# Kernel tuning notes

Measured on AMD Instinct MI355X. Metric: run time of the kernel, lower is better.

## Reference

```python
import jax, jax.numpy as jnp
import numpy as np

B = 16      # number of point clouds
N = 4096    # points per cloud (max after densify)
D = 3       # xyz


def setup_inputs() -> dict:
    key = jax.random.key(0)
    k1, k2 = jax.random.split(key)
    pred = jax.random.normal(k1, (B * N, D), dtype=jnp.float32)
    target = jax.random.normal(k2, (B * N, D), dtype=jnp.float32)
    # sorted segment ids, equal-sized clouds (faithful to to_dense_batch usage)
    batch = jnp.repeat(jnp.arange(B, dtype=jnp.int64), N)
    return {"pred": pred, "target": target, "batch": batch}


def to_dense_batch(x, batch, num_batches, max_n):
    # PyG to_dense_batch: scatter flat points into [B, max_n, D], zero-padded.
    ones = jnp.ones_like(batch)
    counts = jax.ops.segment_sum(ones, batch, num_segments=num_batches)
    offsets = jnp.concatenate([jnp.zeros((1,), batch.dtype), jnp.cumsum(counts)[:-1]])
    pos = jnp.arange(batch.shape[0], dtype=batch.dtype) - offsets[batch]
    dense = jnp.zeros((num_batches, max_n, x.shape[-1]), x.dtype)
    return dense.at[batch, pos].set(x)


def chamfer_distance(x, y):
    # squared-euclidean pairwise distances via the GEMM identity
    x2 = jnp.sum(x * x, axis=-1)                      # [B, N]
    y2 = jnp.sum(y * y, axis=-1)                      # [B, M]
    xy = jnp.einsum('bnd,bmd->bnm', x, y)             # [B, N, M]
    d = x2[:, :, None] + y2[:, None, :] - 2.0 * xy    # [B, N, M]
    cham_x = jnp.mean(jnp.min(d, axis=2), axis=1)     # mean over N of min over M
    cham_y = jnp.mean(jnp.min(d, axis=1), axis=1)     # mean over M of min over N
    # point_reduction='mean', batch_reduction='mean' (pytorch3d defaults)
    return jnp.mean(cham_x + cham_y)


def reference(pred, target, batch):
    x = to_dense_batch(pred, batch, B, N)
    y = to_dense_batch(target, batch, B, N)
    return chamfer_distance(x, y)
```

## Files before the change

kernel.cpp:

```cpp
#include <hip/hip_runtime.h>


namespace {

constexpr int kB = 16;
constexpr int kN = 4096;
constexpr int kPlane = kB * kN;
constexpr int kJS = 2;
constexpr int kJSL = kN / kJS;
constexpr float kScale = 1.0f / (float)(kB * kN);

typedef short bf16x8 __attribute__((ext_vector_type(8)));
typedef float f32x16 __attribute__((ext_vector_type(16)));
typedef unsigned short u16;

__device__ inline u16 bf16_rn(float f) {
  union { float f; unsigned u; } v; v.f = f;
  unsigned r = v.u + 0x7fffu + ((v.u >> 16) & 1u);
  return (u16)(r >> 16);
}
__device__ inline float bf16_f(u16 h) {
  union { unsigned u; float f; } v; v.u = (unsigned)h << 16;
  return v.f;
}
__device__ inline unsigned pk2(u16 lo, u16 hi) {
  return (unsigned)lo | ((unsigned)hi << 16);
}

__global__ void init_out(float* out) { out[0] = 0.0f; }

__global__ __launch_bounds__(256) void cd_prep(
    const float* __restrict__ pred, const float* __restrict__ targ,
    u16* __restrict__ Ab, u16* __restrict__ Bb, float* __restrict__ out) {
  const int p = blockIdx.x * 256 + threadIdx.x;
  if (p == 0) out[0] = 0.0f;
  const u16 one = 0x3F80;
  {
    const float a = pred[3 * p], c = pred[3 * p + 1], d = pred[3 * p + 2];
    const u16 ah = bf16_rn(a), ch = bf16_rn(c), dh = bf16_rn(d);
    const u16 al = bf16_rn(a - bf16_f(ah));
    const u16 cl = bf16_rn(c - bf16_f(ch));
    const u16 dl = bf16_rn(d - bf16_f(dh));
    const float s2 = fmaf(a, a, fmaf(c, c, d * d));
    const u16 s2h = bf16_rn(s2);
    const u16 s2l = bf16_rn(s2 - bf16_f(s2h));
    uint4 w0, w1;
    w0.x = pk2(ah, ch); w0.y = pk2(dh, al); w0.z = pk2(cl, dl); w0.w = pk2(ah, ch);
    w1.x = pk2(dh, s2h); w1.y = pk2(s2l, one); w1.z = pk2(one, al); w1.w = pk2(cl, dl);
    uint4* dst = reinterpret_cast<uint4*>(Ab + (size_t)p * 16);
    dst[0] = w0; dst[1] = w1;
  }
  {
    const float a = targ[3 * p], c = targ[3 * p + 1], d = targ[3 * p + 2];
    const u16 ah0 = bf16_rn(a), ch0 = bf16_rn(c), dh0 = bf16_rn(d);
    const u16 ah = bf16_rn(-2.0f * bf16_f(ah0));
    const u16 ch = bf16_rn(-2.0f * bf16_f(ch0));
    const u16 dh = bf16_rn(-2.0f * bf16_f(dh0));
    const u16 al = bf16_rn(-2.0f * bf16_f(bf16_rn(a - bf16_f(ah0))));
    const u16 cl = bf16_rn(-2.0f * bf16_f(bf16_rn(c - bf16_f(ch0))));
    const u16 dl = bf16_rn(-2.0f * bf16_f(bf16_rn(d - bf16_f(dh0))));
    const float s2 = fmaf(a, a, fmaf(c, c, d * d));
    const u16 s2h = bf16_rn(s2);
    const u16 s2l = bf16_rn(s2 - bf16_f(s2h));
    uint4 w0, w1;
    w0.x = pk2(ah, ch); w0.y = pk2(dh, ah); w0.z = pk2(ch, dh); w0.w = pk2(al, cl);
    w1.x = pk2(dl, one); w1.y = pk2(one, s2h); w1.z = pk2(s2l, al); w1.w = pk2(cl, dl);
    uint4* dst = reinterpret_cast<uint4*>(Bb + (size_t)p * 16);
    dst[0] = w0; dst[1] = w1;
  }
}

__global__ __launch_bounds__(256) void cd_rowmin(
    const u16* __restrict__ Ab, const u16* __restrict__ Bb,
    float* __restrict__ rowpart) {
  const int t = threadIdx.x;
  const int w = t >> 6, lane = t & 63;
  const int half = lane >> 5, l31 = lane & 31;
  const int chunk = blockIdx.x;
  const int cloud = blockIdx.y;
  const int z = blockIdx.z;
  const int dir = z / kJS;
  const int slice = z % kJS;

  const u16* __restrict__ RowM = dir ? Bb : Ab;
  const u16* __restrict__ ColM = dir ? Ab : Bb;

  const int arow = cloud * kN + chunk * 128 + w * 32 + l31;
  const bf16x8 afrag = *(const bf16x8*)(RowM + (size_t)arow * 16 + half * 8);

  f32x16 zacc;
#pragma unroll
  for (int r = 0; r < 16; ++r) zacc[r] = 0.0f;
  float rmin[16];
#pragma unroll
  for (int r = 0; r < 16; ++r) rmin[r] = 1e30f;

  const u16* bbase = ColM + ((size_t)cloud * kN + slice * kJSL) * 16;
  constexpr int NT = kJSL / 64;
  const int jcol = l31 * 16 + half * 8;
#pragma unroll 2
  for (int jt = 0; jt < NT; ++jt) {
    const u16* bp = bbase + jt * 64 * 16;
    const bf16x8 b0 = *(const bf16x8*)(bp + jcol);
    const bf16x8 b1 = *(const bf16x8*)(bp + 32 * 16 + jcol);
    const f32x16 s0 = __builtin_amdgcn_mfma_f32_32x32x16_bf16(afrag, b0, zacc, 0, 0, 0);
    const f32x16 s1 = __builtin_amdgcn_mfma_f32_32x32x16_bf16(afrag, b1, zacc, 0, 0, 0);
#pragma unroll
    for (int r = 0; r < 16; ++r)
      rmin[r] = fminf(rmin[r], fminf(s0[r], s1[r]));
  }

#pragma unroll
  for (int st = 1; st < 32; st <<= 1) {
#pragma unroll
    for (int r = 0; r < 16; ++r)
      rmin[r] = fminf(rmin[r], __shfl_xor(rmin[r], st, 64));
  }
  if (l31 == 0) {
    float* rp = rowpart + ((size_t)z * kB + cloud) * kN + chunk * 128 + w * 32;
#pragma unroll
    for (int r = 0; r < 16; ++r) {
      const int row = (r & 3) + 8 * (r >> 2) + 4 * half;
      rp[row] = rmin[r];
    }
  }
}

__global__ __launch_bounds__(256) void cd_reduce(
    const float* __restrict__ rowpart, float* __restrict__ out) {
  const int u = blockIdx.x * 256 + threadIdx.x;
  const int dir = u >> 16, rest = u & (kPlane - 1);
  const int cloud = rest >> 12, p = rest & (kN - 1);
  float rm = 1e30f;
#pragma unroll
  for (int s2 = 0; s2 < kJS; ++s2)
    rm = fminf(rm, rowpart[(((size_t)(dir * kJS + s2)) * kB + cloud) * kN + p]);
  float s = rm;
  for (int o = 32; o > 0; o >>= 1) s += __shfl_down(s, o, 64);
  __shared__ float wsum[4];
  const int lane = threadIdx.x & 63, wv = threadIdx.x >> 6;
  if (lane == 0) wsum[wv] = s;
  __syncthreads();
  if (threadIdx.x == 0)
    atomicAdd(out, (wsum[0] + wsum[1] + wsum[2] + wsum[3]) * kScale);
}

template <int KX>
__global__ __launch_bounds__(256) void chamfer_direct(
    const float* __restrict__ pred, const float* __restrict__ targ,
    float* __restrict__ out) {
  __shared__ float4 tA[128], tB[128];
  const int t = threadIdx.x;
  const int xb = blockIdx.x, b = blockIdx.y, dir = blockIdx.z;
  const float* __restrict__ X = dir ? targ : pred;
  const float* __restrict__ Y = dir ? pred : targ;
  float2 xx2[KX], xy2[KX], xz2[KX];
  float x2[KX], mn[KX];
  const int ibase = b * kN + xb * (256 * KX) + t;
#pragma unroll
  for (int k = 0; k < KX; ++k) {
    const int i = ibase + k * 256;
    const float a = X[3 * i], c = X[3 * i + 1], d = X[3 * i + 2];
    x2[k] = fmaf(a, a, fmaf(c, c, d * d));
    xx2[k] = make_float2(-2.0f * a, -2.0f * a);
    xy2[k] = make_float2(-2.0f * c, -2.0f * c);
    xz2[k] = make_float2(-2.0f * d, -2.0f * d);
    mn[k] = 1e30f;
  }
  for (int t0 = 0; t0 < kN; t0 += 256) {
    __syncthreads();
    if (t < 128) {
      const int j0 = 3 * (b * kN + t0 + 2 * t);
      const float a0 = Y[j0], c0 = Y[j0 + 1], d0 = Y[j0 + 2];
      const float a1 = Y[j0 + 3], c1 = Y[j0 + 4], d1 = Y[j0 + 5];
      tA[t] = make_float4(a0, a1, c0, c1);
      tB[t] = make_float4(d0, d1, fmaf(a0, a0, fmaf(c0, c0, d0 * d0)),
                          fmaf(a1, a1, fmaf(c1, c1, d1 * d1)));
    }
    __syncthreads();
    for (int jj = 0; jj < 128; ++jj) {
      const float4 qa = tA[jj], qb = tB[jj];
      const float2 qx = make_float2(qa.x, qa.y), qy = make_float2(qa.z, qa.w);
      const float2 qz = make_float2(qb.x, qb.y), qw = make_float2(qb.z, qb.w);
#pragma unroll
      for (int k = 0; k < KX; ++k) {
        float2 acc;
        asm("v_pk_fma_f32 %0, %1, %2, %3\n\t"
            "v_pk_fma_f32 %0, %4, %5, %0\n\t"
            "v_pk_fma_f32 %0, %6, %7, %0"
            : "=&v"(acc)
            : "v"(xz2[k]), "v"(qz), "v"(qw), "v"(xy2[k]), "v"(qy),
              "v"(xx2[k]), "v"(qx));
        asm("v_min3_f32 %0, %0, %1, %2" : "+v"(mn[k]) : "v"(acc.x), "v"(acc.y));
      }
    }
  }
  float s = 0.0f;
#pragma unroll
  for (int k = 0; k < KX; ++k) s += x2[k] + mn[k];
  for (int o = 32; o > 0; o >>= 1) s += __shfl_down(s, o, 64);
  __shared__ float wsum[4];
  const int lane = t & 63, wv = t >> 6;
  if (lane == 0) wsum[wv] = s;
  __syncthreads();
  if (t == 0)
    atomicAdd(out, (wsum[0] + wsum[1] + wsum[2] + wsum[3]) * kScale);
}

}

extern "C" void kernel_launch(void* const* d_in, const int* in_sizes, int n_in,
                              void* d_out, int out_size, void* d_ws,
                              size_t ws_size, hipStream_t stream) {
  const float* pred = (const float*)d_in[0];
  const float* targ = (const float*)d_in[1];
  float* out = (float*)d_out;

  const size_t needA = (size_t)kPlane * 16 * sizeof(u16);
  const size_t needRow = (size_t)2 * kJS * kPlane * sizeof(float);
  if (ws_size >= 2 * needA + needRow) {
    u16* Ab = (u16*)d_ws;
    u16* Bb = (u16*)((char*)d_ws + needA);
    float* rowpart = (float*)((char*)d_ws + 2 * needA);
    cd_prep<<<dim3(kPlane / 256), 256, 0, stream>>>(pred, targ, Ab, Bb, out);
    cd_rowmin<<<dim3(32, kB, 2 * kJS), 256, 0, stream>>>(Ab, Bb, rowpart);
    cd_reduce<<<dim3(2 * kPlane / 256), 256, 0, stream>>>(rowpart, out);
  } else {
    init_out<<<dim3(1), dim3(1), 0, stream>>>(out);
    constexpr int KX = 8;
    dim3 grid(kN / (256 * KX), kB, 2);
    chamfer_direct<KX><<<grid, 256, 0, stream>>>(pred, targ, out);
  }
}
```

Before: 114.1 us.

## Register-block four A fragments per wave and split columns across waves

Each wave now holds four 32-row A fragments and walks a quarter of the column points, so every B fragment it loads feeds eight MFMAs where it previously fed two. The two-way column slicing across the grid is replaced by a four-way split across the waves of a block, which halves the grid and doubles the rowpart buffer read by the reduce kernel. This cuts global B traffic per MFMA at the cost of 64 accumulator registers of running minima per lane plus MFMA result registers, which may lower occupancy, and the loop-unroll pragma is dropped.

```diff
diff --git a/kernel.cpp b/kernel.cpp
--- a/kernel.cpp
+++ b/kernel.cpp
@@ -6,8 +6,8 @@
 constexpr int kB = 16;
 constexpr int kN = 4096;
 constexpr int kPlane = kB * kN;
-constexpr int kJS = 2;
-constexpr int kJSL = kN / kJS;
+constexpr int kQ = 4;
+constexpr int kQL = kN / kQ;
 constexpr float kScale = 1.0f / (float)(kB * kN);
 
 typedef short bf16x8 __attribute__((ext_vector_type(8)));
@@ -78,51 +78,64 @@
   const int half = lane >> 5, l31 = lane & 31;
   const int chunk = blockIdx.x;
   const int cloud = blockIdx.y;
-  const int z = blockIdx.z;
-  const int dir = z / kJS;
-  const int slice = z % kJS;
+  const int dir = blockIdx.z;
 
   const u16* __restrict__ RowM = dir ? Bb : Ab;
   const u16* __restrict__ ColM = dir ? Ab : Bb;
 
-  const int arow = cloud * kN + chunk * 128 + w * 32 + l31;
-  const bf16x8 afrag = *(const bf16x8*)(RowM + (size_t)arow * 16 + half * 8);
+  bf16x8 af[4];
+#pragma unroll
+  for (int a = 0; a < 4; ++a) {
+    const int arow = cloud * kN + chunk * 128 + a * 32 + l31;
+    af[a] = *(const bf16x8*)(RowM + (size_t)arow * 16 + half * 8);
+  }
 
   f32x16 zacc;
 #pragma unroll
   for (int r = 0; r < 16; ++r) zacc[r] = 0.0f;
-  float rmin[16];
-#pragma unroll
-  for (int r = 0; r < 16; ++r) rmin[r] = 1e30f;
-
-  const u16* bbase = ColM + ((size_t)cloud * kN + slice * kJSL) * 16;
-  constexpr int NT = kJSL / 64;
+  float rmin[4][16];
+#pragma unroll
+  for (int a = 0; a < 4; ++a)
+#pragma unroll
+    for (int r = 0; r < 16; ++r) rmin[a][r] = 1e30f;
+
+  const u16* bbase = ColM + ((size_t)cloud * kN + w * kQL) * 16;
+  constexpr int NT = kQL / 64;
   const int jcol = l31 * 16 + half * 8;
-#pragma unroll 2
   for (int jt = 0; jt < NT; ++jt) {
     const u16* bp = bbase + jt * 64 * 16;
     const bf16x8 b0 = *(const bf16x8*)(bp + jcol);
     const bf16x8 b1 = *(const bf16x8*)(bp + 32 * 16 + jcol);
-    const f32x16 s0 = __builtin_amdgcn_mfma_f32_32x32x16_bf16(afrag, b0, zacc, 0, 0, 0);
-    const f32x16 s1 = __builtin_amdgcn_mfma_f32_32x32x16_bf16(afrag, b1, zacc, 0, 0, 0);
-#pragma unroll
-    for (int r = 0; r < 16; ++r)
-      rmin[r] = fminf(rmin[r], fminf(s0[r], s1[r]));
+#pragma unroll
+    for (int a = 0; a < 4; ++a) {
+      const f32x16 s0 =
+          __builtin_amdgcn_mfma_f32_32x32x16_bf16(af[a], b0, zacc, 0, 0, 0);
+      const f32x16 s1 =
+          __builtin_amdgcn_mfma_f32_32x32x16_bf16(af[a], b1, zacc, 0, 0, 0);
+#pragma unroll
+      for (int r = 0; r < 16; ++r)
+        rmin[a][r] = fminf(rmin[a][r], fminf(s0[r], s1[r]));
+    }
   }
 
 #pragma unroll
   for (int st = 1; st < 32; st <<= 1) {
 #pragma unroll
-    for (int r = 0; r < 16; ++r)
-      rmin[r] = fminf(rmin[r], __shfl_xor(rmin[r], st, 64));
+    for (int a = 0; a < 4; ++a)
+#pragma unroll
+      for (int r = 0; r < 16; ++r)
+        rmin[a][r] = fminf(rmin[a][r], __shfl_xor(rmin[a][r], st, 64));
   }
   if (l31 == 0) {
-    float* rp = rowpart + ((size_t)z * kB + cloud) * kN + chunk * 128 + w * 32;
-#pragma unroll
-    for (int r = 0; r < 16; ++r) {
-      const int row = (r & 3) + 8 * (r >> 2) + 4 * half;
-      rp[row] = rmin[r];
-    }
+    float* rp =
+        rowpart + (((size_t)dir * kQ + w) * kB + cloud) * kN + chunk * 128;
+#pragma unroll
+    for (int a = 0; a < 4; ++a)
+#pragma unroll
+      for (int r = 0; r < 16; ++r) {
+        const int row = (r & 3) + 8 * (r >> 2) + 4 * half;
+        rp[a * 32 + row] = rmin[a][r];
+      }
   }
 }
 
@@ -133,8 +146,8 @@
   const int cloud = rest >> 12, p = rest & (kN - 1);
   float rm = 1e30f;
 #pragma unroll
-  for (int s2 = 0; s2 < kJS; ++s2)
-    rm = fminf(rm, rowpart[(((size_t)(dir * kJS + s2)) * kB + cloud) * kN + p]);
+  for (int q = 0; q < kQ; ++q)
+    rm = fminf(rm, rowpart[(((size_t)dir * kQ + q) * kB + cloud) * kN + p]);
   float s = rm;
   for (int o = 32; o > 0; o >>= 1) s += __shfl_down(s, o, 64);
   __shared__ float wsum[4];
@@ -217,13 +230,13 @@
   float* out = (float*)d_out;
 
   const size_t needA = (size_t)kPlane * 16 * sizeof(u16);
-  const size_t needRow = (size_t)2 * kJS * kPlane * sizeof(float);
+  const size_t needRow = (size_t)2 * kQ * kPlane * sizeof(float);
   if (ws_size >= 2 * needA + needRow) {
     u16* Ab = (u16*)d_ws;
     u16* Bb = (u16*)((char*)d_ws + needA);
     float* rowpart = (float*)((char*)d_ws + 2 * needA);
     cd_prep<<<dim3(kPlane / 256), 256, 0, stream>>>(pred, targ, Ab, Bb, out);
-    cd_rowmin<<<dim3(32, kB, 2 * kJS), 256, 0, stream>>>(Ab, Bb, rowpart);
+    cd_rowmin<<<dim3(32, kB, 2), 256, 0, stream>>>(Ab, Bb, rowpart);
     cd_reduce<<<dim3(2 * kPlane / 256), 256, 0, stream>>>(rowpart, out);
   } else {
     init_out<<<dim3(1), dim3(1), 0, stream>>>(out);
```

Measured after the change: 112.0 us. No clear change (-1.9%).
